# Performance work log

Hardware: AMD Instinct MI355X
Metric: run time of the kernel (lower is better)

Reference implementation:

```python
import jax, jax.numpy as jnp
import numpy as np

NUM_CLASSES = 21
POS_T, NEG_T, ALPHA, GAMMA, EPS = 0.5, 0.4, 0.25, 2.0, 1e-6
NEG_FILL = -1e30  # sorts below any focal value (focal >= 0)


def _pairwise_iou(a, b):
    # a: [A,4], b: [T,4] -> [A,T]
    x1 = jnp.maximum(a[:, None, 0], b[None, :, 0])
    y1 = jnp.maximum(a[:, None, 1], b[None, :, 1])
    x2 = jnp.minimum(a[:, None, 2], b[None, :, 2])
    y2 = jnp.minimum(a[:, None, 3], b[None, :, 3])
    inter = jnp.clip(x2 - x1, 0) * jnp.clip(y2 - y1, 0)
    a1 = (a[:, 2] - a[:, 0]) * (a[:, 3] - a[:, 1])
    a2 = (b[:, 2] - b[:, 0]) * (b[:, 3] - b[:, 1])
    return inter / (a1[:, None] + a2[None, :] - inter + EPS)


def _giou_loss(b1, b2):
    # b1, b2: [N,4] -> [N]
    x1 = jnp.maximum(b1[:, 0], b2[:, 0]); y1 = jnp.maximum(b1[:, 1], b2[:, 1])
    x2 = jnp.minimum(b1[:, 2], b2[:, 2]); y2 = jnp.minimum(b1[:, 3], b2[:, 3])
    inter = jnp.clip(x2 - x1, 0) * jnp.clip(y2 - y1, 0)
    a1 = (b1[:, 2] - b1[:, 0]) * (b1[:, 3] - b1[:, 1])
    a2 = (b2[:, 2] - b2[:, 0]) * (b2[:, 3] - b2[:, 1])
    union = a1 + a2 - inter
    iou = inter / (union + EPS)
    ex1 = jnp.minimum(b1[:, 0], b2[:, 0]); ey1 = jnp.minimum(b1[:, 1], b2[:, 1])
    ex2 = jnp.maximum(b1[:, 2], b2[:, 2]); ey2 = jnp.maximum(b1[:, 3], b2[:, 3])
    enc = (ex2 - ex1) * (ey2 - ey1)
    giou = iou - (enc - union) / (enc + EPS)
    return 1.0 - giou


def _per_image(conf, bbox, tb, tl, anchors):
    # conf: [A,C], bbox: [A,4], tb: [T,4], tl: [T], anchors: [A,4]
    A, C = conf.shape
    ious = _pairwise_iou(anchors, tb)                 # [A,T]
    max_ious = ious.max(axis=1)
    best_t = jnp.argmax(ious, axis=1)                 # [A] best target per anchor
    pos = max_ious >= POS_T
    neg = max_ious < NEG_T
    best_a = jnp.argmax(ious, axis=0)                 # [T] force-match best anchor per GT
    pos = pos.at[best_a].set(True)
    neg = neg.at[best_a].set(False)

    conf_target = jax.nn.one_hot(tl[best_t], C, dtype=conf.dtype) * pos[:, None].astype(conf.dtype)
    probs = jax.nn.softmax(conf, axis=1)
    is_pos_cell = conf_target == 1.0
    pt = jnp.where(is_pos_cell, probs, 1.0 - probs)
    alpha_f = jnp.where(is_pos_cell, ALPHA, 1.0 - ALPHA)
    focal = -alpha_f * (1.0 - pt) ** GAMMA * jnp.log(jnp.clip(pt, EPS))  # [A,C]

    num_pos = pos.sum()
    n_neg = neg.sum()
    pos_sum = jnp.where(pos[:, None], focal, 0.0).sum()

    # hard-negative mining: descending sort of masked flattened focal, sum top-k
    neg_flat = jnp.where(neg[:, None], focal, NEG_FILL).reshape(-1)
    sorted_neg = jnp.sort(neg_flat)[::-1]
    idx = jnp.arange(neg_flat.shape[0])
    k = jnp.minimum(3 * num_pos, n_neg)
    topk_sum = jnp.where(idx < k, sorted_neg, 0.0).sum()
    denom = jnp.maximum(num_pos + k, 1).astype(conf.dtype)
    conf_pos = jnp.where(n_neg > 0, (pos_sum + topk_sum) / denom,
                         pos_sum / jnp.maximum(num_pos, 1).astype(conf.dtype))

    k2 = jnp.minimum(100, n_neg)
    top2_mean = jnp.where(idx < k2, sorted_neg, 0.0).sum() / jnp.maximum(k2, 1).astype(conf.dtype)
    conf_nopos = jnp.where(n_neg > 0, top2_mean, focal.mean())
    conf_loss = jnp.where(num_pos > 0, conf_pos, conf_nopos)

    matched = tb[best_t]                              # [A,4]
    giou_l = _giou_loss(bbox, matched)                # [A]
    d = bbox - matched
    ad = jnp.abs(d)
    l1 = jnp.where(ad < 1.0, 0.5 * d * d, ad - 0.5).mean(axis=1)
    per = giou_l + 0.5 * l1
    bbox_loss = jnp.where(num_pos > 0,
                          jnp.where(pos, per, 0.0).sum() / jnp.maximum(num_pos, 1).astype(conf.dtype),
                          0.0)
    return conf_loss, bbox_loss


def _loss(conf_pred, bbox_pred, anchors, target_boxes, target_labels):
    conf_l, bbox_l = jax.vmap(
        lambda c, b, tb, tl: _per_image(c, b, tb, tl, anchors)
    )(conf_pred, bbox_pred, target_boxes, target_labels)
    conf_loss = conf_l.mean()
    bbox_loss = bbox_l.mean()
    total = 1.0 * conf_loss + 1.0 * bbox_loss  # conf_weight = bbox_weight = 1.0
    return jnp.stack([total, conf_loss, bbox_loss])


def _rand_boxes(key, shape):
    k1, k2 = jax.random.split(key)
    xy1 = jax.random.uniform(k1, shape + (2,)) * 0.8
    wh = jax.random.uniform(k2, shape + (2,)) * 0.2 + 0.01
    return jnp.concatenate([xy1, xy1 + wh], axis=-1)


def setup_inputs() -> dict:
    key = jax.random.key(0)
    ks = jax.random.split(key, 5)
    B, A, T, C = 16, 65536, 32, NUM_CLASSES
    conf_pred = jax.random.normal(ks[0], (B, A, C), dtype=jnp.float32)
    bbox_pred = _rand_boxes(ks[1], (B, A))
    anchors = _rand_boxes(ks[2], (A,))
    target_boxes = _rand_boxes(ks[3], (B, T))
    target_labels = jax.random.randint(ks[4], (B, T), 1, C)
    return {"conf_pred": conf_pred, "bbox_pred": bbox_pred, "anchors": anchors,
            "target_boxes": target_boxes, "target_labels": target_labels}


def reference(conf_pred, bbox_pred, anchors, target_boxes, target_labels):
    return _loss(conf_pred, bbox_pred, anchors, target_boxes, target_labels)
```

## Files before the change

### kernel.cpp

```cpp
#include <hip/hip_runtime.h>


#define AN 65536
#define BN 16
#define TN 32
#define CN 21
#define NBA 2048
#define LCAPG (2 * 65536)
#define LCAP 10240
#define CHUNK 256
#define BUFC (CHUNK * CN)

struct BlockAcc { float pos_sum; float bbox_sum; unsigned np; unsigned nn; };
struct ImgParams { double pos; double bbox; unsigned np, nn, k, ve, act; };

__device__ __forceinline__ float box_area(float4 B) {
    return __fmul_rn(__fsub_rn(B.z, B.x), __fsub_rn(B.w, B.y));
}
__device__ __forceinline__ float iou_rcp(float4 A, float aa, float4 T, float ta) {
    float x1 = fmaxf(A.x, T.x), y1 = fmaxf(A.y, T.y);
    float x2 = fminf(A.z, T.z), y2 = fminf(A.w, T.w);
    float inter = __fmul_rn(fmaxf(__fsub_rn(x2, x1), 0.f), fmaxf(__fsub_rn(y2, y1), 0.f));
    float den = __fadd_rn(__fsub_rn(__fadd_rn(aa, ta), inter), 1e-6f);
    return __fmul_rn(inter, __builtin_amdgcn_rcpf(den));
}
__device__ __forceinline__ float row_prep(const float* __restrict__ row, float* __restrict__ c) {
#pragma unroll
    for (int j = 0; j < CN; ++j) c[j] = row[j];
    float m1[10];
#pragma unroll
    for (int j = 0; j < 10; ++j) m1[j] = fmaxf(c[j], c[j + 10]);
    float m2[5];
#pragma unroll
    for (int j = 0; j < 5; ++j) m2[j] = fmaxf(m1[j], m1[j + 5]);
    float ma = fmaxf(m2[0], m2[1]), mb = fmaxf(m2[2], m2[3]);
    float m = fmaxf(fmaxf(ma, mb), fmaxf(m2[4], c[20]));
#pragma unroll
    for (int j = 0; j < CN; ++j) c[j] = __expf(__fsub_rn(c[j], m));
    float s1[10];
#pragma unroll
    for (int j = 0; j < 10; ++j) s1[j] = __fadd_rn(c[j], c[j + 10]);
    float s2[5];
#pragma unroll
    for (int j = 0; j < 5; ++j) s2[j] = __fadd_rn(s1[j], s1[j + 5]);
    float sa = __fadd_rn(s2[0], s2[1]), sb = __fadd_rn(s2[2], s2[3]);
    float s = __fadd_rn(__fadd_rn(sa, sb), __fadd_rn(s2[4], c[20]));
    return __builtin_amdgcn_rcpf(s);
}
__device__ __forceinline__ float cell_focal(float cexp, float inv, bool cellpos) {
    float p = __fmul_rn(cexp, inv);
    float pt = cellpos ? p : __fsub_rn(1.0f, p);
    float af = cellpos ? 0.25f : 0.75f;
    float om = __fsub_rn(1.0f, pt);
    float lg = __logf(fmaxf(pt, 1e-6f));
    return __fmul_rn(__fmul_rn(__fmul_rn(-af, om), om), lg);
}
__device__ __forceinline__ unsigned focal_bits(float fo) {
    unsigned bits = __float_as_uint(fo);
    if (bits == 0x80000000u) bits = 0u;
    return bits;
}
__device__ __forceinline__ float bbox_per(float4 b1, float4 b2) {
    float x1 = fmaxf(b1.x, b2.x), y1 = fmaxf(b1.y, b2.y);
    float x2 = fminf(b1.z, b2.z), y2 = fminf(b1.w, b2.w);
    float inter = fmaxf(x2 - x1, 0.f) * fmaxf(y2 - y1, 0.f);
    float a1 = (b1.z - b1.x) * (b1.w - b1.y);
    float a2 = (b2.z - b2.x) * (b2.w - b2.y);
    float un = a1 + a2 - inter;
    float iou = inter / (un + 1e-6f);
    float ex1 = fminf(b1.x, b2.x), ey1 = fminf(b1.y, b2.y);
    float ex2 = fmaxf(b1.z, b2.z), ey2 = fmaxf(b1.w, b2.w);
    float enc = (ex2 - ex1) * (ey2 - ey1);
    float giou = iou - (enc - un) / (enc + 1e-6f);
    float gl = 1.0f - giou;
    float l1 = 0.f, d, ad;
    d = b1.x - b2.x; ad = fabsf(d); l1 += (ad < 1.f) ? (0.5f * d * d) : (ad - 0.5f);
    d = b1.y - b2.y; ad = fabsf(d); l1 += (ad < 1.f) ? (0.5f * d * d) : (ad - 0.5f);
    d = b1.z - b2.z; ad = fabsf(d); l1 += (ad < 1.f) ? (0.5f * d * d) : (ad - 0.5f);
    d = b1.w - b2.w; ad = fabsf(d); l1 += (ad < 1.f) ? (0.5f * d * d) : (ad - 0.5f);
    return gl + 0.5f * (l1 * 0.25f);
}
__device__ __forceinline__ unsigned mbcnt64(unsigned long long m) {
    return __builtin_amdgcn_mbcnt_hi((unsigned)(m >> 32),
           __builtin_amdgcn_mbcnt_lo((unsigned)m, 0u));
}

__global__ __launch_bounds__(256) void main_kernel(
    const float* __restrict__ conf, const float4* __restrict__ bboxp,
    const float4* __restrict__ anchors, const float4* __restrict__ tboxes,
    const int* __restrict__ tlabels,
    unsigned long long* __restrict__ gbest,
    unsigned* __restrict__ ahist, unsigned* __restrict__ maxb,
    BlockAcc* __restrict__ blockAcc)
{
    __shared__ float4 tbS[TN];
    __shared__ int tlS[TN];
    __shared__ float taS[TN];
    __shared__ float iouS[TN][260];
    __shared__ unsigned ahp[NBA / 2];
    __shared__ float pbV[TN][8];
    __shared__ int   pbA[TN][8];
    __shared__ float rF[2][4];
    __shared__ unsigned rI[2][4];
    int b = blockIdx.y, tid = threadIdx.x;
    int a = blockIdx.x * 256 + tid;
    for (int i = tid; i < NBA / 2; i += 256) ahp[i] = 0u;
    if (tid < TN) {
        float4 T = tboxes[b * TN + tid];
        tbS[tid] = T; tlS[tid] = tlabels[b * TN + tid]; taS[tid] = box_area(T);
    }
    float4 ab = anchors[a];
    float aa = box_area(ab);
    __syncthreads();

    float best = -1.0f; int bt = 0;
#pragma unroll
    for (int t = 0; t < TN; ++t) {
        float iou = iou_rcp(ab, aa, tbS[t], taS[t]);
        iouS[t][tid] = iou;
        if (iou > best) { best = iou; bt = t; }
    }
    __syncthreads();

    {
        int t = tid & 31, pp = tid >> 5;
        const float4* rp = (const float4*)(&iouS[t][pp * 32]);
        float bv = -1.f; int ba = 0;
#pragma unroll
        for (int q = 0; q < 8; ++q) {
            float4 v4 = rp[q];
            int i0 = pp * 32 + q * 4;
            if (v4.x > bv) { bv = v4.x; ba = i0 + 0; }
            if (v4.y > bv) { bv = v4.y; ba = i0 + 1; }
            if (v4.z > bv) { bv = v4.z; ba = i0 + 2; }
            if (v4.w > bv) { bv = v4.w; ba = i0 + 3; }
        }
        pbV[t][pp] = bv; pbA[t][pp] = ba;
    }
    __syncthreads();
    if (tid < TN) {
        float bv = -1.f; int ba = 0;
#pragma unroll
        for (int pp = 0; pp < 8; ++pp) {
            float v = pbV[tid][pp];
            if (v > bv) { bv = v; ba = pbA[tid][pp]; }
        }
        unsigned ga = blockIdx.x * 256 + (unsigned)ba;
        unsigned long long key =
            (((unsigned long long)__float_as_uint(bv)) << 32) | (unsigned long long)(unsigned)(~ga);
        atomicMax(&gbest[b * TN + tid], key);
    }

    size_t idx = (size_t)b * AN + a;
    bool posA = best >= 0.5f;
    bool negA = best < 0.4f;
    float fs = 0.f, bper = 0.f;
    unsigned mbenc = 0u;
    if (posA || negA) {
        float c[CN];
        float inv = row_prep(conf + idx * CN, c);
        if (posA) {
            int label = tlS[bt];
#pragma unroll
            for (int j = 0; j < CN; ++j) fs += cell_focal(c[j], inv, j == label);
            bper = bbox_per(bboxp[idx], tbS[bt]);
        } else {
            float m1[10];
#pragma unroll
            for (int j = 0; j < 10; ++j) m1[j] = fmaxf(c[j], c[j + 10]);
            float m2[5];
#pragma unroll
            for (int j = 0; j < 5; ++j) m2[j] = fmaxf(m1[j], m1[j + 5]);
            float ma = fmaxf(m2[0], m2[1]), mb2 = fmaxf(m2[2], m2[3]);
            float cmax = fmaxf(fmaxf(ma, mb2), fmaxf(m2[4], c[20]));
            float fo = cell_focal(cmax, inv, false);
            unsigned mb = focal_bits(fo);
            mbenc = (mb << 1) | 1u;
            unsigned bin = mb >> 20;
            atomicAdd(&ahp[bin >> 1], 1u << ((bin & 1) << 4));
        }
    }
    maxb[idx] = mbenc;

    float vpos = posA ? fs : 0.f, vb = bper;
    unsigned inp = posA ? 1u : 0u, inn = negA ? 1u : 0u;
#pragma unroll
    for (int off = 32; off; off >>= 1) {
        vpos += __shfl_down(vpos, off, 64);
        vb   += __shfl_down(vb,   off, 64);
        inp  += __shfl_down(inp,  off, 64);
        inn  += __shfl_down(inn,  off, 64);
    }
    int wv = tid >> 6, ln = tid & 63;
    if (ln == 0) { rF[0][wv] = vpos; rF[1][wv] = vb; rI[0][wv] = inp; rI[1][wv] = inn; }
    __syncthreads();
    if (tid == 0) {
        BlockAcc ba2;
        ba2.pos_sum = rF[0][0] + rF[0][1] + rF[0][2] + rF[0][3];
        ba2.bbox_sum = rF[1][0] + rF[1][1] + rF[1][2] + rF[1][3];
        ba2.np = rI[0][0] + rI[0][1] + rI[0][2] + rI[0][3];
        ba2.nn = rI[1][0] + rI[1][1] + rI[1][2] + rI[1][3];
        blockAcc[b * 256 + blockIdx.x] = ba2;
    }
    for (int i = tid; i < NBA / 2; i += 256) {
        unsigned v = ahp[i];
        if (v) {
            if (v & 0xFFFFu) atomicAdd(&ahist[b * NBA + 2 * i], v & 0xFFFFu);
            if (v >> 16)     atomicAdd(&ahist[b * NBA + 2 * i + 1], v >> 16);
        }
    }
}

__global__ __launch_bounds__(1024) void tailA_kernel(
    const float* __restrict__ conf, const float4* __restrict__ bboxp,
    const float4* __restrict__ anchors, const float4* __restrict__ tboxes,
    const int* __restrict__ tlabels,
    const unsigned long long* __restrict__ gbest,
    const BlockAcc* __restrict__ blockAcc,
    const unsigned* __restrict__ ahist, unsigned* __restrict__ maxb,
    ImgParams* __restrict__ params)
{
    __shared__ unsigned hist[NBA];
    __shared__ unsigned scan_[1024];
    __shared__ unsigned gaS[TN];
    __shared__ float4 tbS[TN];
    __shared__ int tlS[TN];
    __shared__ float taS[TN];
    __shared__ float dps[TN], dbb[TN];
    __shared__ int dnp[TN], dnn[TN];
    __shared__ double sdbl[16];
    __shared__ unsigned suns[16];
    __shared__ double s_pos, s_bbox;
    __shared__ unsigned s_np, s_nn, s_k, s_act, s_ve;

    int b = blockIdx.x, tid = threadIdx.x;
    int wv = tid >> 6, ln = tid & 63;

    for (int i = tid; i < NBA; i += 1024) hist[i] = ahist[b * NBA + i];
    if (tid < TN) {
        gaS[tid] = ~(unsigned)(gbest[b * TN + tid] & 0xFFFFFFFFull);
        float4 T = tboxes[b * TN + tid];
        tbS[tid] = T; tlS[tid] = tlabels[b * TN + tid]; taS[tid] = box_area(T);
        dps[tid] = 0.f; dbb[tid] = 0.f; dnp[tid] = 0; dnn[tid] = 0;
    }
    __syncthreads();

    if (tid < TN) {
        bool doit = true;
        unsigned ga = gaS[tid];
        for (int u = 0; u < tid; ++u) if (gaS[u] == ga) doit = false;
        if (doit) {
            size_t idx = (size_t)b * AN + ga;
            float4 ab = anchors[ga];
            float aa = box_area(ab);
            float best = -1.f; int bt = 0;
#pragma unroll
            for (int t = 0; t < TN; ++t) {
                float iou = iou_rcp(ab, aa, tbS[t], taS[t]);
                if (iou > best) { best = iou; bt = t; }
            }
            if (best < 0.5f) {
                int label = tlS[bt];
                float c[CN];
                float inv = row_prep(conf + idx * CN, c);
                float fsv = 0.f;
#pragma unroll
                for (int j = 0; j < CN; ++j) fsv += cell_focal(c[j], inv, j == label);
                dps[tid] = fsv;
                dbb[tid] = bbox_per(bboxp[idx], tbS[bt]);
                dnp[tid] = 1;
                if (best < 0.4f) {
                    unsigned enc = maxb[idx];
                    atomicSub(&hist[enc >> 21], 1u);
                    maxb[idx] = 0u;
                    dnn[tid] = -1;
                }
            }
        }
    }
    __syncthreads();

    if (tid < 256) {
        BlockAcc ba = blockAcc[b * 256 + tid];
        double ps = (double)ba.pos_sum, bs = (double)ba.bbox_sum;
        unsigned np = ba.np, nn = ba.nn;
#pragma unroll
        for (int off = 32; off; off >>= 1) {
            ps += __shfl_down(ps, off, 64);
            bs += __shfl_down(bs, off, 64);
            np += __shfl_down(np, off, 64);
            nn += __shfl_down(nn, off, 64);
        }
        if (ln == 0) { sdbl[wv] = ps; sdbl[8 + wv] = bs; suns[wv] = np; suns[8 + wv] = nn; }
    }
    __syncthreads();
    if (tid == 0) {
        double dp = 0, db = 0; int cp = 0, cn = 0;
        for (int i = 0; i < TN; ++i) { dp += dps[i]; db += dbb[i]; cp += dnp[i]; cn += dnn[i]; }
        s_pos = sdbl[0] + sdbl[1] + sdbl[2] + sdbl[3] + dp;
        s_bbox = sdbl[8] + sdbl[9] + sdbl[10] + sdbl[11] + db;
        unsigned NP = (unsigned)((int)(suns[0] + suns[1] + suns[2] + suns[3]) + cp);
        unsigned NN = (unsigned)((int)(suns[8] + suns[9] + suns[10] + suns[11]) + cn);
        s_np = NP; s_nn = NN;
        unsigned k = min(3u * NP, NN);
        s_k = k;
        s_act = (NN > 0 && k > 0) ? 1u : 0u;
        s_ve = 0u;
    }
    __syncthreads();

    if (s_act) {
        unsigned k = s_k;
        unsigned lc0 = hist[tid * 2], lc1 = hist[tid * 2 + 1];
        unsigned cc = lc0 + lc1;
        scan_[tid] = cc;
        __syncthreads();
        for (int off = 1; off < 1024; off <<= 1) {
            unsigned v = (tid + off < 1024) ? scan_[tid + off] : 0u;
            __syncthreads();
            scan_[tid] += v;
            __syncthreads();
        }
        {
            unsigned above = (tid < 1023) ? scan_[tid + 1] : 0u;
            if (above < k && above + cc >= k) {
                unsigned bin = (above + lc1 >= k) ? (unsigned)(tid * 2 + 1) : (unsigned)(tid * 2);
                s_ve = (bin << 21) | 1u;
            }
        }
        __syncthreads();
    }
    if (tid == 0) {
        ImgParams P;
        P.pos = s_pos; P.bbox = s_bbox;
        P.np = s_np; P.nn = s_nn; P.k = s_k; P.ve = s_ve; P.act = s_act;
        params[b] = P;
    }
}

__global__ __launch_bounds__(256) void tailB_kernel(
    const float* __restrict__ conf, const unsigned* __restrict__ maxb,
    const ImgParams* __restrict__ params,
    float* __restrict__ list, unsigned* __restrict__ listCnt)
{
    __shared__ int candS[1024];
    __shared__ unsigned bufS[BUFC];
    __shared__ unsigned s_cnt, s_bcnt, s_gbase;
    int b = blockIdx.y, tid = threadIdx.x;
    unsigned act = params[b].act;
    if (!act) return;
    unsigned ve = params[b].ve;
    unsigned vbits = ve >> 1;
    int base = blockIdx.x * 1024;

    if (tid == 0) s_cnt = 0u;
    __syncthreads();

    const uint4* mb4 = (const uint4*)(maxb + (size_t)b * AN + base);
    uint4 m4 = mb4[tid];
    unsigned c0 = (m4.x >= ve), c1 = (m4.y >= ve), c2 = (m4.z >= ve), c3 = (m4.w >= ve);
    unsigned cnt = c0 + c1 + c2 + c3;
    unsigned pos = 0;
    if (cnt) pos = atomicAdd(&s_cnt, cnt);
    int a0 = base + tid * 4;
    if (c0) candS[pos++] = a0 + 0;
    if (c1) candS[pos++] = a0 + 1;
    if (c2) candS[pos++] = a0 + 2;
    if (c3) candS[pos++] = a0 + 3;
    __syncthreads();
    unsigned n = s_cnt;

    for (unsigned cbase = 0; cbase < n; cbase += CHUNK) {
        if (tid == 0) s_bcnt = 0u;
        __syncthreads();
        unsigned i = cbase + tid;
        if (i < n) {
            int a = candS[i];
            size_t idx = (size_t)b * AN + a;
            float c[CN];
            float inv = row_prep(conf + idx * CN, c);
#pragma unroll
            for (int j = 0; j < CN; ++j) {
                float fo = cell_focal(c[j], inv, false);
                unsigned bits = focal_bits(fo);
                bool hit = bits >= vbits;
                unsigned long long msk = __ballot(hit);
                if (hit) {
                    unsigned pre = mbcnt64(msk);
                    unsigned bb = 0;
                    if (pre == 0) bb = atomicAdd(&s_bcnt, (unsigned)__popcll(msk));
                    bb = __shfl(bb, (int)(__ffsll((long long)msk) - 1), 64);
                    bufS[bb + pre] = bits;
                }
            }
        }
        __syncthreads();
        unsigned ccnt = s_bcnt;
        if (ccnt) {
            if (tid == 0) s_gbase = atomicAdd(&listCnt[b * 16], ccnt);
            __syncthreads();
            unsigned gb = s_gbase;
            for (unsigned j2 = tid; j2 < ccnt; j2 += 256) {
                unsigned p = gb + j2;
                if (p < (unsigned)LCAPG)
                    list[(size_t)b * LCAPG + p] = __uint_as_float(bufS[j2]);
            }
        }
        __syncthreads();
    }
}

__global__ __launch_bounds__(1024) void tailC_kernel(
    const float* __restrict__ list, const unsigned* __restrict__ listCnt,
    const ImgParams* __restrict__ params,
    double* __restrict__ imgRes, unsigned* __restrict__ ctr,
    float* __restrict__ out)
{
    __shared__ float lcache[LCAP];
    __shared__ unsigned hist[4096];
    __shared__ unsigned scan_[1024];
    __shared__ double sdbl[16];
    __shared__ double s_sumAbove;
    __shared__ unsigned s_b1, s_rem, s_b2, s_rem2, s_b3, s_rem3;

    int b = blockIdx.x, tid = threadIdx.x;
    int wv = tid >> 6, ln = tid & 63;
    ImgParams P = params[b];
    double topk = 0.0;

    if (P.act) {
        unsigned n = min(listCnt[b * 16], (unsigned)LCAPG);
        const float* gl = list + (size_t)b * LCAPG;
        bool inL = (n <= (unsigned)LCAP);
        if (inL) for (unsigned i = tid; i < n; i += 1024) lcache[i] = gl[i];
        if (tid == 0) { s_b1 = 0; s_rem = 0; s_b3 = 0; s_rem3 = 0; }
        for (int i = tid; i < 4096; i += 1024) hist[i] = 0u;
        __syncthreads();

        for (unsigned i = tid; i < n; i += 1024) {
            unsigned bits = __float_as_uint(inL ? lcache[i] : gl[i]);
            atomicAdd(&hist[bits >> 20], 1u);
        }
        __syncthreads();

        unsigned lc0 = hist[tid * 2], lc1 = hist[tid * 2 + 1];
        unsigned cc = lc0 + lc1;
        scan_[tid] = cc;
        __syncthreads();
        for (int off = 1; off < 1024; off <<= 1) {
            unsigned v = (tid + off < 1024) ? scan_[tid + off] : 0u;
            __syncthreads();
            scan_[tid] += v;
            __syncthreads();
        }
        {
            unsigned total = scan_[0];
            unsigned above = (tid < 1023) ? scan_[tid + 1] : 0u;
            unsigned r = min(P.k, total);
            if (r > 0 && above < r && above + cc >= r) {
                if (above + lc1 >= r) { s_b1 = (unsigned)(tid * 2 + 1); s_rem = r - above; }
                else { s_b1 = (unsigned)(tid * 2); s_rem = r - above - lc1; }
            }
        }
        __syncthreads();
        unsigned b1 = s_b1, rem = s_rem;

        for (int i = tid; i < 4096; i += 1024) hist[i] = 0u;
        __syncthreads();
        double sA = 0.0;
        for (unsigned i = tid; i < n; i += 1024) {
            float v = inL ? lcache[i] : gl[i];
            unsigned bits = __float_as_uint(v);
            unsigned hi = bits >> 20;
            if (hi > b1) sA += (double)v;
            else if (hi == b1) atomicAdd(&hist[(bits >> 8) & 0xFFFu], 1u);
        }
#pragma unroll
        for (int off = 32; off; off >>= 1) sA += __shfl_down(sA, off, 64);
        if (ln == 0) sdbl[wv] = sA;
        __syncthreads();
        if (tid == 0) {
            double tt = 0;
            for (int w = 0; w < 16; ++w) tt += sdbl[w];
            s_sumAbove = tt;
        }
        __syncthreads();
        double sumAbove = s_sumAbove;

        if (rem == 0) {
            topk = sumAbove;
        } else {
            unsigned l4[4], cc4 = 0;
#pragma unroll
            for (int q = 0; q < 4; ++q) { l4[q] = hist[tid * 4 + q]; cc4 += l4[q]; }
            scan_[tid] = cc4;
            __syncthreads();
            for (int off = 1; off < 1024; off <<= 1) {
                unsigned v = (tid + off < 1024) ? scan_[tid + off] : 0u;
                __syncthreads();
                scan_[tid] += v;
                __syncthreads();
            }
            {
                unsigned total = scan_[0];
                unsigned above = (tid < 1023) ? scan_[tid + 1] : 0u;
                unsigned r = min(rem, total);
                if (above < r && above + cc4 >= r) {
                    unsigned a2 = above;
                    for (int i = 3; i >= 0; --i) {
                        unsigned bc = l4[i];
                        if (a2 + bc >= r) { s_b2 = (unsigned)(tid * 4 + i); s_rem2 = r - a2; break; }
                        a2 += bc;
                    }
                }
            }
            __syncthreads();
            unsigned b2 = s_b2, rem2 = s_rem2;
            if (tid < 256) hist[tid] = 0u;
            __syncthreads();

            double sMid = 0.0;
            for (unsigned i = tid; i < n; i += 1024) {
                float v = inL ? lcache[i] : gl[i];
                unsigned bits = __float_as_uint(v);
                if ((bits >> 20) != b1) continue;
                unsigned sub = (bits >> 8) & 0xFFFu;
                if (sub > b2) sMid += (double)v;
                else if (sub == b2) atomicAdd(&hist[bits & 0xFFu], 1u);
            }
            __syncthreads();
            if (tid < 256) scan_[tid] = hist[tid];
            __syncthreads();
            for (int off = 1; off < 256; off <<= 1) {
                unsigned v = 0;
                if (tid < 256 && tid + off < 256) v = scan_[tid + off];
                __syncthreads();
                if (tid < 256) scan_[tid] += v;
                __syncthreads();
            }
            if (tid < 256) {
                unsigned above8 = (tid < 255) ? scan_[tid + 1] : 0u;
                unsigned c8 = hist[tid];
                if (above8 < rem2 && above8 + c8 >= rem2) { s_b3 = (unsigned)tid; s_rem3 = rem2 - above8; }
            }
            __syncthreads();
            unsigned b3 = s_b3, rem3 = s_rem3;

            double s3 = 0.0;
            for (unsigned i = tid; i < n; i += 1024) {
                float v = inL ? lcache[i] : gl[i];
                unsigned bits = __float_as_uint(v);
                if ((bits >> 20) == b1 && ((bits >> 8) & 0xFFFu) == b2 && (bits & 0xFFu) > b3)
                    s3 += (double)v;
            }
            double tot = sMid + s3;
#pragma unroll
            for (int off = 32; off; off >>= 1) tot += __shfl_down(tot, off, 64);
            if (ln == 0) sdbl[wv] = tot;
            __syncthreads();
            if (tid == 0) {
                double totAll = 0;
                for (int w = 0; w < 16; ++w) totAll += sdbl[w];
                unsigned vb3 = (b1 << 20) | (b2 << 8) | b3;
                topk = sumAbove + totAll + (double)rem3 * (double)__uint_as_float(vb3);
            }
        }
    }

    if (tid == 0) {
        double confl;
        if (P.act) confl = (P.pos + topk) / (double)max(P.np + P.k, 1u);
        else       confl = P.pos / (double)max(P.np, 1u);
        imgRes[b * 2 + 0] = confl;
        imgRes[b * 2 + 1] = P.bbox / (double)max(P.np, 1u);
        __threadfence();
        unsigned prev = atomicAdd(ctr, 1u);
        if (prev == BN - 1) {
            __threadfence();
            double cs = 0, bs = 0;
            for (int i = 0; i < BN; ++i) { cs += imgRes[i * 2]; bs += imgRes[i * 2 + 1]; }
            cs /= BN; bs /= BN;
            out[0] = (float)(cs + bs);
            out[1] = (float)cs;
            out[2] = (float)bs;
        }
    }
}

extern "C" void kernel_launch(void* const* d_in, const int* in_sizes, int n_in,
                              void* d_out, int out_size, void* d_ws, size_t ws_size,
                              hipStream_t stream)
{
    (void)in_sizes; (void)n_in; (void)out_size; (void)ws_size;
    const float*  conf    = (const float*)d_in[0];
    const float4* bboxp   = (const float4*)d_in[1];
    const float4* anchors = (const float4*)d_in[2];
    const float4* tboxes  = (const float4*)d_in[3];
    const int*    tlabels = (const int*)d_in[4];
    float* out = (float*)d_out;
    char* ws = (char*)d_ws;
    size_t off = 0;
    auto alloc = [&](size_t bytes) -> void* {
        void* p = (void*)(ws + off);
        off = (off + bytes + 255) & ~(size_t)255;
        return p;
    };
    unsigned*  maxb     = (unsigned*)alloc((size_t)BN * AN * 4);
    float*     list     = (float*)alloc((size_t)BN * LCAPG * 4);
    BlockAcc*  blockAcc = (BlockAcc*)alloc((size_t)BN * 256 * sizeof(BlockAcc));
    double*    imgRes   = (double*)alloc((size_t)BN * 2 * 8);
    ImgParams* params   = (ImgParams*)alloc((size_t)BN * sizeof(ImgParams));
    size_t zstart = off;
    unsigned long long* gbest = (unsigned long long*)alloc((size_t)BN * TN * 8);
    unsigned* ahist   = (unsigned*)alloc((size_t)BN * NBA * 4);
    unsigned* ctr     = (unsigned*)alloc(256);
    unsigned* listCnt = (unsigned*)alloc((size_t)BN * 16 * 4);
    size_t zbytes = off - zstart;
    hipMemsetAsync(ws + zstart, 0, zbytes, stream);

    dim3 gridA(AN / 256, BN);
    main_kernel<<<gridA, 256, 0, stream>>>(conf, bboxp, anchors, tboxes, tlabels,
                                           gbest, ahist, maxb, blockAcc);
    tailA_kernel<<<BN, 1024, 0, stream>>>(conf, bboxp, anchors, tboxes, tlabels,
                                          gbest, blockAcc, ahist, maxb, params);
    tailB_kernel<<<dim3(64, BN), 256, 0, stream>>>(conf, maxb, params, list, listCnt);
    tailC_kernel<<<BN, 1024, 0, stream>>>(list, listCnt, params, imgRes, ctr, out);
}
```

Before: 204.7 us.

## Stage conf rows through shared memory with coalesced float4 loads, reusing IoU buffer

The block's 256x21 conf tile is now loaded cooperatively as coalesced float4 reads into shared memory, replacing strided 21-float per-thread row loads. The buffer is shared with the IoU staging array, so the IoU argmax pass is split into two 16-target halves to fit, adding extra barriers. The negative-anchor max recomputation is dropped because the exp of the max logit minus itself is 1. The tile is now loaded for every anchor, including ignored ones, and the stride-21 shared reads may cause bank conflicts.

```diff
diff --git a/kernel.cpp b/kernel.cpp
--- a/kernel.cpp
+++ b/kernel.cpp
@@ -24,9 +24,7 @@
     float den = __fadd_rn(__fsub_rn(__fadd_rn(aa, ta), inter), 1e-6f);
     return __fmul_rn(inter, __builtin_amdgcn_rcpf(den));
 }
-__device__ __forceinline__ float row_prep(const float* __restrict__ row, float* __restrict__ c) {
-#pragma unroll
-    for (int j = 0; j < CN; ++j) c[j] = row[j];
+__device__ __forceinline__ float row_prep_vals(float* __restrict__ c) {
     float m1[10];
 #pragma unroll
     for (int j = 0; j < 10; ++j) m1[j] = fmaxf(c[j], c[j + 10]);
@@ -46,6 +44,11 @@
     float sa = __fadd_rn(s2[0], s2[1]), sb = __fadd_rn(s2[2], s2[3]);
     float s = __fadd_rn(__fadd_rn(sa, sb), __fadd_rn(s2[4], c[20]));
     return __builtin_amdgcn_rcpf(s);
+}
+__device__ __forceinline__ float row_prep(const float* __restrict__ row, float* __restrict__ c) {
+#pragma unroll
+    for (int j = 0; j < CN; ++j) c[j] = row[j];
+    return row_prep_vals(c);
 }
 __device__ __forceinline__ float cell_focal(float cexp, float inv, bool cellpos) {
     float p = __fmul_rn(cexp, inv);
@@ -96,7 +99,7 @@
     __shared__ float4 tbS[TN];
     __shared__ int tlS[TN];
     __shared__ float taS[TN];
-    __shared__ float iouS[TN][260];
+    __shared__ float uS[5376];
     __shared__ unsigned ahp[NBA / 2];
     __shared__ float pbV[TN][8];
     __shared__ int   pbA[TN][8];
@@ -115,29 +118,32 @@
 
     float best = -1.0f; int bt = 0;
 #pragma unroll
-    for (int t = 0; t < TN; ++t) {
-        float iou = iou_rcp(ab, aa, tbS[t], taS[t]);
-        iouS[t][tid] = iou;
-        if (iou > best) { best = iou; bt = t; }
-    }
-    __syncthreads();
-
-    {
-        int t = tid & 31, pp = tid >> 5;
-        const float4* rp = (const float4*)(&iouS[t][pp * 32]);
-        float bv = -1.f; int ba = 0;
-#pragma unroll
-        for (int q = 0; q < 8; ++q) {
-            float4 v4 = rp[q];
-            int i0 = pp * 32 + q * 4;
-            if (v4.x > bv) { bv = v4.x; ba = i0 + 0; }
-            if (v4.y > bv) { bv = v4.y; ba = i0 + 1; }
-            if (v4.z > bv) { bv = v4.z; ba = i0 + 2; }
-            if (v4.w > bv) { bv = v4.w; ba = i0 + 3; }
-        }
-        pbV[t][pp] = bv; pbA[t][pp] = ba;
-    }
-    __syncthreads();
+    for (int h = 0; h < 2; ++h) {
+#pragma unroll
+        for (int t2 = 0; t2 < 16; ++t2) {
+            int t = h * 16 + t2;
+            float iou = iou_rcp(ab, aa, tbS[t], taS[t]);
+            uS[t2 * 260 + tid] = iou;
+            if (iou > best) { best = iou; bt = t; }
+        }
+        __syncthreads();
+        if (tid < 128) {
+            int t2 = tid & 15, pp = tid >> 4;
+            const float4* rp = (const float4*)&uS[t2 * 260 + pp * 32];
+            float bv = -1.f; int ba = 0;
+#pragma unroll
+            for (int q = 0; q < 8; ++q) {
+                float4 v4 = rp[q];
+                int i0 = pp * 32 + q * 4;
+                if (v4.x > bv) { bv = v4.x; ba = i0 + 0; }
+                if (v4.y > bv) { bv = v4.y; ba = i0 + 1; }
+                if (v4.z > bv) { bv = v4.z; ba = i0 + 2; }
+                if (v4.w > bv) { bv = v4.w; ba = i0 + 3; }
+            }
+            pbV[h * 16 + t2][pp] = bv; pbA[h * 16 + t2][pp] = ba;
+        }
+        __syncthreads();
+    }
     if (tid < TN) {
         float bv = -1.f; int ba = 0;
 #pragma unroll
@@ -150,6 +156,13 @@
             (((unsigned long long)__float_as_uint(bv)) << 32) | (unsigned long long)(unsigned)(~ga);
         atomicMax(&gbest[b * TN + tid], key);
     }
+
+    {
+        const float4* cb4 = (const float4*)(conf + ((size_t)b * AN + (size_t)blockIdx.x * 256) * CN);
+        float4* u4 = (float4*)uS;
+        for (int i = tid; i < 1344; i += 256) u4[i] = cb4[i];
+    }
+    __syncthreads();
 
     size_t idx = (size_t)b * AN + a;
     bool posA = best >= 0.5f;
@@ -158,22 +171,16 @@
     unsigned mbenc = 0u;
     if (posA || negA) {
         float c[CN];
-        float inv = row_prep(conf + idx * CN, c);
+#pragma unroll
+        for (int j = 0; j < CN; ++j) c[j] = uS[tid * CN + j];
+        float inv = row_prep_vals(c);
         if (posA) {
             int label = tlS[bt];
 #pragma unroll
             for (int j = 0; j < CN; ++j) fs += cell_focal(c[j], inv, j == label);
             bper = bbox_per(bboxp[idx], tbS[bt]);
         } else {
-            float m1[10];
-#pragma unroll
-            for (int j = 0; j < 10; ++j) m1[j] = fmaxf(c[j], c[j + 10]);
-            float m2[5];
-#pragma unroll
-            for (int j = 0; j < 5; ++j) m2[j] = fmaxf(m1[j], m1[j + 5]);
-            float ma = fmaxf(m2[0], m2[1]), mb2 = fmaxf(m2[2], m2[3]);
-            float cmax = fmaxf(fmaxf(ma, mb2), fmaxf(m2[4], c[20]));
-            float fo = cell_focal(cmax, inv, false);
+            float fo = cell_focal(1.0f, inv, false);
             unsigned mb = focal_bits(fo);
             mbenc = (mb << 1) | 1u;
             unsigned bin = mb >> 20;
```

Result: slower. 215.9 us (+5.5%).
